# Kernel tuning notes

Hardware: AMD Instinct MI355X
Metric: run time of the kernel (lower is better)

Reference implementation:

```python
import jax, jax.numpy as jnp
import numpy as np

N, CIN, COUT, H, CH, K, M = 60000, 128, 128, 8, 16, 27, 960000


def setup_inputs() -> dict:
    key = jax.random.key(0)
    ks = jax.random.split(key, 12)
    f32 = jnp.float32
    s = 1.0 / np.sqrt(CIN)
    return {
        "feats": jax.random.normal(ks[0], (N, CIN), f32),
        "norm_points": jax.random.uniform(ks[1], (N, 3), f32) - 0.5,
        "w1": jax.random.normal(ks[2], (3, 3), f32) * 0.5,
        "bn1_scale": jnp.ones((3,), f32),
        "bn1_shift": jnp.zeros((3,), f32),
        "w2": jax.random.normal(ks[3], (3, CIN), f32) * 0.5,
        "bn2_scale": jnp.ones((CIN,), f32),
        "bn2_shift": jnp.zeros((CIN,), f32),
        "w3": jax.random.normal(ks[4], (CIN, CIN), f32) * s,
        "b3": jnp.zeros((CIN,), f32),
        "wq": jax.random.normal(ks[5], (CIN, COUT), f32) * s,
        "bq": jnp.zeros((COUT,), f32),
        "wv": jax.random.normal(ks[6], (CIN, COUT), f32) * s,
        "bv": jnp.zeros((COUT,), f32),
        "wo": jax.random.normal(ks[7], (COUT, COUT), f32) * s,
        "bo": jnp.zeros((COUT,), f32),
        "pos_enc": jax.random.normal(ks[8], (K, H, CH), f32),
        # kq_map row0 = key_idx * K + kernel_offset; row1 = query_idx
        "kq_row0": jax.random.randint(ks[9], (M,), 0, N * K, dtype=jnp.int32).astype(jnp.int64),
        "kq_row1": jax.random.randint(ks[10], (M,), 0, N, dtype=jnp.int32).astype(jnp.int64),
    }


def _l2norm(x):
    # F.normalize(p=2, dim=-1) with eps clamp
    n = jnp.linalg.norm(x, axis=-1, keepdims=True)
    return x / jnp.maximum(n, 1e-12)


def reference(feats, norm_points, w1, bn1_scale, bn1_shift, w2, bn2_scale, bn2_shift,
              w3, b3, wq, bq, wv, bv, wo, bo, pos_enc, kq_row0, kq_row1):
    # intra-voxel positional MLP (BN folded to eval-mode scale/shift)
    h = jax.nn.relu((norm_points @ w1) * bn1_scale + bn1_shift)
    h = jax.nn.relu((h @ w2) * bn2_scale + bn2_shift)
    x = feats + (h @ w3 + b3)                      # [N, CIN]

    q = (x @ wq + bq).reshape(N, H, CH)            # [N, H, CH]
    v = (x @ wv + bv).reshape(N, H, CH)

    nq = _l2norm(q)                                # normalized queries
    npos = _l2norm(pos_enc)                        # [K, H, CH]

    koff = kq_row0 % K                             # kernel-offset index into pos_enc
    kidx = kq_row0 // K                            # key (value) index

    # dot_product_cuda: attn[m,h] = <nq[query_m], npos[offset_m]>
    attn = jnp.einsum('mhc,mhc->mh', nq[kq_row1], npos[koff])   # [M, H]

    # scalar_attention_cuda: out[query_m] += attn[m] * v[key_m]
    msg = attn[:, :, None] * v[kidx]                             # [M, H, CH]
    out = jax.ops.segment_sum(msg, kq_row1, num_segments=N)      # [N, H, CH]

    return out.reshape(N, COUT) @ wo + bo
```

## Files before the change

### kernel.cpp

```cpp
#include <hip/hip_runtime.h>
#include <hip/hip_bf16.h>

#define NPTS  60000
#define KK    27
#define NEDGE 960000
#define CAP   96

typedef __attribute__((ext_vector_type(8))) short bf16x8;
typedef __attribute__((ext_vector_type(4))) float f32x4;

__device__ __forceinline__ unsigned short f2bf(float x) {
    unsigned u = __float_as_uint(x);
    return (unsigned short)((u + 0x7FFFu + ((u >> 16) & 1u)) >> 16);
}

union U8 { bf16x8 v; unsigned u[4]; };

__device__ __forceinline__ void split8(float4 a, float4 b, bf16x8& hi, bf16x8& lo) {
    float av[8] = {a.x, a.y, a.z, a.w, b.x, b.y, b.z, b.w};
    U8 h, l;
#pragma unroll
    for (int p = 0; p < 4; ++p) {
        float x0 = av[2 * p], x1 = av[2 * p + 1];
        unsigned hp;
        asm("v_cvt_pk_bf16_f32 %0, %1, %2" : "=v"(hp) : "v"(x0), "v"(x1));
        float hf0 = __uint_as_float(hp << 16);
        float hf1 = __uint_as_float(hp & 0xFFFF0000u);
        float r0 = x0 - hf0, r1 = x1 - hf1;
        unsigned lp;
        asm("v_cvt_pk_bf16_f32 %0, %1, %2" : "=v"(lp) : "v"(r0), "v"(r1));
        h.u[p] = hp; l.u[p] = lp;
    }
    hi = h.v; lo = l.v;
}

__global__ __launch_bounds__(256) void tiny_mlp_kernel(
    const float* __restrict__ npnts,
    const float* __restrict__ w1, const float* __restrict__ bn1s, const float* __restrict__ bn1h,
    const float* __restrict__ w2, const float* __restrict__ bn2s, const float* __restrict__ bn2h,
    float* __restrict__ h2out) {
    __shared__ float w2s[3 * 128];
    __shared__ float sc2[128], sh2[128];
    __shared__ float w1s[9], sc1[3], sh1[3];
    __shared__ float h2s[64 * 129];

    const int tid = threadIdx.x;
    for (int i = tid; i < 384; i += 256) w2s[i] = w2[i];
    if (tid < 128) { sc2[tid] = bn2s[tid]; sh2[tid] = bn2h[tid]; }
    if (tid < 9) w1s[tid] = w1[tid];
    if (tid < 3) { sc1[tid] = bn1s[tid]; sh1[tid] = bn1h[tid]; }
    __syncthreads();

    const int p  = tid >> 2;
    const int cq = (tid & 3) * 32;
    const int pt = blockIdx.x * 64 + p;
    float h1a = 0.f, h1b = 0.f, h1c = 0.f;
    if (pt < NPTS) {
        float p0 = npnts[pt * 3 + 0], p1 = npnts[pt * 3 + 1], p2 = npnts[pt * 3 + 2];
        float t0 = p0 * w1s[0] + p1 * w1s[3] + p2 * w1s[6];
        float t1 = p0 * w1s[1] + p1 * w1s[4] + p2 * w1s[7];
        float t2 = p0 * w1s[2] + p1 * w1s[5] + p2 * w1s[8];
        h1a = fmaxf(t0 * sc1[0] + sh1[0], 0.f);
        h1b = fmaxf(t1 * sc1[1] + sh1[1], 0.f);
        h1c = fmaxf(t2 * sc1[2] + sh1[2], 0.f);
    }
    for (int c = cq; c < cq + 32; ++c) {
        float t = h1a * w2s[c] + h1b * w2s[128 + c] + h1c * w2s[256 + c];
        h2s[p * 129 + c] = fmaxf(t * sc2[c] + sh2[c], 0.f);
    }
    __syncthreads();
    for (int i = tid; i < 64 * 128; i += 256) {
        int row = i >> 7, col = i & 127;
        int gr = blockIdx.x * 64 + row;
        if (gr < NPTS) h2out[gr * 128 + col] = h2s[row * 129 + col];
    }
}

__global__ __launch_bounds__(256) void pack_w_kernel(
    const float* __restrict__ w3, const float* __restrict__ wq,
    const float* __restrict__ wv, const float* __restrict__ wo,
    short* __restrict__ hi, short* __restrict__ lo) {
    const float* srcs[4] = {w3, wq, wv, wo};
    const float* w = srcs[blockIdx.y];
    short* whi = hi + blockIdx.y * 16384;
    short* wlo = lo + blockIdx.y * 16384;
    int base = (blockIdx.x * 256 + threadIdx.x) * 4;
#pragma unroll
    for (int j = 0; j < 4; ++j) {
        int o   = base + j;
        int s   = o & 7;
        int c16 = (o >> 3) & 15;
        int q   = (o >> 7) & 3;
        int t   = (o >> 9) & 7;
        int ks  = (o >> 12) & 3;
        float x = w[(ks * 32 + q * 8 + s) * 128 + (t * 16 + c16)];
        unsigned short h = f2bf(x);
        float hf = __uint_as_float((unsigned)h << 16);
        whi[o] = (short)h;
        wlo[o] = (short)f2bf(x - hf);
    }
}

template <int MODE>
__global__ __launch_bounds__(256, 2) void mfma_gemm_kernel(
    const float* __restrict__ in,
    const short* __restrict__ whi_g, const short* __restrict__ wlo_g,
    const float* __restrict__ bias, const float* __restrict__ resid,
    float* __restrict__ out) {
    const int tid  = threadIdx.x;
    const int lane = tid & 63;
    const int wv   = tid >> 6;
    const int q    = lane >> 4;
    const int cl   = lane & 15;
    const int rowbase = blockIdx.x * 128 + wv * 32;

    const bf16x8* BH = (const bf16x8*)whi_g;
    const bf16x8* BL = (const bf16x8*)wlo_g;
    const float* inA0 = &in[(size_t)min(rowbase + cl,      NPTS - 1) * 128];
    const float* inA1 = &in[(size_t)min(rowbase + 16 + cl, NPTS - 1) * 128];

    f32x4 acc[2][8];
#pragma unroll
    for (int u = 0; u < 2; ++u)
#pragma unroll
        for (int t = 0; t < 8; ++t) acc[u][t] = (f32x4){0.f, 0.f, 0.f, 0.f};

#pragma unroll
    for (int ks = 0; ks < 4; ++ks) {
        float4 a0a = *(const float4*)&inA0[ks * 32 + q * 8];
        float4 a0b = *(const float4*)&inA0[ks * 32 + q * 8 + 4];
        float4 a1a = *(const float4*)&inA1[ks * 32 + q * 8];
        float4 a1b = *(const float4*)&inA1[ks * 32 + q * 8 + 4];
        bf16x8 ah0, al0, ah1, al1;
        split8(a0a, a0b, ah0, al0);
        split8(a1a, a1b, ah1, al1);
#pragma unroll
        for (int t = 0; t < 8; ++t) {
            const int fi = ((ks * 8 + t) * 4 + q) * 16 + cl;
            bf16x8 bh = BH[fi];
            bf16x8 bl = BL[fi];
            acc[0][t] = __builtin_amdgcn_mfma_f32_16x16x32_bf16(ah0, bh, acc[0][t], 0, 0, 0);
            acc[0][t] = __builtin_amdgcn_mfma_f32_16x16x32_bf16(al0, bh, acc[0][t], 0, 0, 0);
            acc[0][t] = __builtin_amdgcn_mfma_f32_16x16x32_bf16(ah0, bl, acc[0][t], 0, 0, 0);
            acc[1][t] = __builtin_amdgcn_mfma_f32_16x16x32_bf16(ah1, bh, acc[1][t], 0, 0, 0);
            acc[1][t] = __builtin_amdgcn_mfma_f32_16x16x32_bf16(al1, bh, acc[1][t], 0, 0, 0);
            acc[1][t] = __builtin_amdgcn_mfma_f32_16x16x32_bf16(ah1, bl, acc[1][t], 0, 0, 0);
        }
    }

    float breg[8];
#pragma unroll
    for (int t = 0; t < 8; ++t) breg[t] = bias[t * 16 + cl];

#pragma unroll
    for (int u = 0; u < 2; ++u) {
#pragma unroll
        for (int t = 0; t < 8; ++t) {
#pragma unroll
            for (int r = 0; r < 4; ++r) {
                int row = rowbase + u * 16 + q * 4 + r;
                float o = acc[u][t][r] + breg[t];
                if (MODE == 1) {
                    if (row < NPTS) o += resid[row * 128 + t * 16 + cl];
                }
                if (MODE == 2) {
                    float ss = o * o;
                    ss += __shfl_xor(ss, 1);
                    ss += __shfl_xor(ss, 2);
                    ss += __shfl_xor(ss, 4);
                    ss += __shfl_xor(ss, 8);
                    o *= 1.f / fmaxf(sqrtf(ss), 1e-12f);
                }
                if (row < NPTS) out[row * 128 + t * 16 + cl] = o;
            }
        }
    }
}

__global__ __launch_bounds__(256) void zero_cnt_kernel(int* __restrict__ cnt) {
    int i = blockIdx.x * 256 + threadIdx.x;
    if (i < NPTS) cnt[i] = 0;
}

__global__ __launch_bounds__(256) void build_buckets_kernel(
    const int* __restrict__ r0, const int* __restrict__ r1,
    int* __restrict__ cnt, int* __restrict__ bucket) {
    int m = blockIdx.x * 256 + threadIdx.x;
    if (m >= NEDGE) return;
    int a = r0[m];
    int q = r1[m];
    if (q < 0 || q >= NPTS) return;
    if (a < 0 || a >= NPTS * KK) return;
    int kidx = a / KK;
    int koff = a - kidx * KK;
    int slot = atomicAdd(&cnt[q], 1);
    if (slot < CAP) bucket[q * CAP + slot] = (kidx << 5) | koff;
}

__global__ __launch_bounds__(256, 8) void attn_scatter_kernel(
    const float* __restrict__ nq, const float* __restrict__ v,
    const float* __restrict__ pos_enc, const int* __restrict__ cnt,
    const int* __restrict__ bucket, float* __restrict__ pre) {
    __shared__ float nps[KK * 128];

    const int tid = threadIdx.x;
    if (tid < KK * 8) {
        const float4* pv = (const float4*)&pos_enc[tid * 16];
        float4 a = pv[0], b = pv[1], c = pv[2], d = pv[3];
        float ss = a.x*a.x + a.y*a.y + a.z*a.z + a.w*a.w
                 + b.x*b.x + b.y*b.y + b.z*b.z + b.w*b.w
                 + c.x*c.x + c.y*c.y + c.z*c.z + c.w*c.w
                 + d.x*d.x + d.y*d.y + d.z*d.z + d.w*d.w;
        float inv = 1.f / fmaxf(sqrtf(ss), 1e-12f);
        float4* o = (float4*)&nps[tid * 16];
        o[0] = make_float4(a.x*inv, a.y*inv, a.z*inv, a.w*inv);
        o[1] = make_float4(b.x*inv, b.y*inv, b.z*inv, b.w*inv);
        o[2] = make_float4(c.x*inv, c.y*inv, c.z*inv, c.w*inv);
        o[3] = make_float4(d.x*inv, d.y*inv, d.z*inv, d.w*inv);
    }
    __syncthreads();

    const int l = tid & 63;
    const int wid = blockIdx.x * 4 + (tid >> 6);
    const int nwaves = gridDim.x * 4;

#define ATT_EDGE(REC) do {                                                  \
        int koff_ = (REC) & 31; int kidx_ = (REC) >> 5;                     \
        float2 np_ = *(const float2*)&nps[koff_ * 128 + 2 * l];             \
        float2 v_  = *(const float2*)&v[kidx_ * 128 + 2 * l];               \
        float a_ = nq2.x * np_.x + nq2.y * np_.y;                           \
        a_ += __shfl_xor(a_, 1); a_ += __shfl_xor(a_, 2);                   \
        a_ += __shfl_xor(a_, 4);                                            \
        accx = fmaf(a_, v_.x, accx); accy = fmaf(a_, v_.y, accy);           \
    } while (0)

    for (int n = wid; n < NPTS; n += nwaves) {
        float2 nq2 = *(const float2*)&nq[n * 128 + 2 * l];
        int deg = min(cnt[n], CAP);
        int base = n * CAP;
        int myrec = (l < deg) ? bucket[base + l] : 0;
        float accx = 0.f, accy = 0.f;
        int dmain = min(deg, 64);
        int e = 0;
        for (; e + 4 <= dmain; e += 4) {
            int r0 = __shfl(myrec, e);
            int r1 = __shfl(myrec, e + 1);
            int r2 = __shfl(myrec, e + 2);
            int r3 = __shfl(myrec, e + 3);
            ATT_EDGE(r0); ATT_EDGE(r1); ATT_EDGE(r2); ATT_EDGE(r3);
        }
        for (; e < dmain; ++e) {
            int r = __shfl(myrec, e);
            ATT_EDGE(r);
        }
        for (; e < deg; ++e) {
            int r = bucket[base + e];
            ATT_EDGE(r);
        }
        *(float2*)&pre[n * 128 + 2 * l] = make_float2(accx, accy);
    }
#undef ATT_EDGE
}

extern "C" void kernel_launch(void* const* d_in, const int* in_sizes, int n_in,
                              void* d_out, int out_size, void* d_ws, size_t ws_size,
                              hipStream_t stream) {
    const float* feats = (const float*)d_in[0];
    const float* npnts = (const float*)d_in[1];
    const float* w1    = (const float*)d_in[2];
    const float* bn1s  = (const float*)d_in[3];
    const float* bn1h  = (const float*)d_in[4];
    const float* w2    = (const float*)d_in[5];
    const float* bn2s  = (const float*)d_in[6];
    const float* bn2h  = (const float*)d_in[7];
    const float* w3    = (const float*)d_in[8];
    const float* b3    = (const float*)d_in[9];
    const float* wq    = (const float*)d_in[10];
    const float* bq    = (const float*)d_in[11];
    const float* wv    = (const float*)d_in[12];
    const float* bv    = (const float*)d_in[13];
    const float* wo    = (const float*)d_in[14];
    const float* bo    = (const float*)d_in[15];
    const float* pos   = (const float*)d_in[16];
    const int*   r0    = (const int*)d_in[17];
    const int*   r1    = (const int*)d_in[18];
    float* out = (float*)d_out;

    float* h2buf = (float*)d_ws;
    float* xbuf  = h2buf + (size_t)NPTS * 128;
    float* nqbuf = xbuf  + (size_t)NPTS * 128;
    float* vbuf  = nqbuf + (size_t)NPTS * 128;
    short* whi_g = (short*)(vbuf + (size_t)NPTS * 128);
    short* wlo_g = whi_g + 4 * 16384;
    float* prebuf = xbuf;
    int*   cnt    = (int*)h2buf;
    int*   bucket = cnt + NPTS;

    dim3 blk(256);
    const int nb64  = (NPTS + 63) / 64;
    const int nb128 = (NPTS + 127) / 128;

    pack_w_kernel<<<dim3(16, 4), blk, 0, stream>>>(w3, wq, wv, wo, whi_g, wlo_g);
    tiny_mlp_kernel<<<nb64, blk, 0, stream>>>(npnts, w1, bn1s, bn1h, w2, bn2s, bn2h, h2buf);
    mfma_gemm_kernel<1><<<nb128, blk, 0, stream>>>(h2buf, whi_g,             wlo_g,             b3, feats, xbuf);
    mfma_gemm_kernel<2><<<nb128, blk, 0, stream>>>(xbuf,  whi_g + 16384,     wlo_g + 16384,     bq, nullptr, nqbuf);
    mfma_gemm_kernel<0><<<nb128, blk, 0, stream>>>(xbuf,  whi_g + 2 * 16384, wlo_g + 2 * 16384, bv, nullptr, vbuf);
    zero_cnt_kernel<<<(NPTS + 255) / 256, blk, 0, stream>>>(cnt);
    build_buckets_kernel<<<(NEDGE + 255) / 256, blk, 0, stream>>>(r0, r1, cnt, bucket);
    attn_scatter_kernel<<<2048, blk, 0, stream>>>(nqbuf, vbuf, pos, cnt, bucket, prebuf);
    mfma_gemm_kernel<0><<<nb128, blk, 0, stream>>>(prebuf, whi_g + 3 * 16384, wlo_g + 3 * 16384, bo, nullptr, out);
}
```

Measured before the change: 387.4 us.

## Fuse positional MLP into x GEMM, merge q/v GEMMs, combine prep kernels

The positional MLP now writes its output into shared memory and feeds the residual GEMM in the same kernel, so the h2 intermediate no longer round-trips through global memory. The q and v projections become one kernel that reads x once and computes both outputs. Weight packing and count zeroing are merged into a single prep launch, which removes launches and re-reads of x in exchange for more registers per thread in the combined q/v kernel.

```diff
diff --git a/kernel.cpp b/kernel.cpp
--- a/kernel.cpp
+++ b/kernel.cpp
@@ -34,15 +34,50 @@
     hi = h.v; lo = l.v;
 }
 
-__global__ __launch_bounds__(256) void tiny_mlp_kernel(
+__global__ __launch_bounds__(256) void prep_kernel(
+    const float* __restrict__ w3, const float* __restrict__ wq,
+    const float* __restrict__ wv, const float* __restrict__ wo,
+    short* __restrict__ hi, short* __restrict__ lo, int* __restrict__ cnt) {
+    const int b = blockIdx.x;
+    const int tid = threadIdx.x;
+    if (b < 64) {
+        const float* srcs[4] = {w3, wq, wv, wo};
+        const int mat = b >> 4;
+        const float* w = srcs[mat];
+        short* whi = hi + mat * 16384;
+        short* wlo = lo + mat * 16384;
+        int base = ((b & 15) * 256 + tid) * 4;
+#pragma unroll
+        for (int j = 0; j < 4; ++j) {
+            int o   = base + j;
+            int s   = o & 7;
+            int c16 = (o >> 3) & 15;
+            int q   = (o >> 7) & 3;
+            int t   = (o >> 9) & 7;
+            int ks  = (o >> 12) & 3;
+            float x = w[(ks * 32 + q * 8 + s) * 128 + (t * 16 + c16)];
+            unsigned short h = f2bf(x);
+            float hf = __uint_as_float((unsigned)h << 16);
+            whi[o] = (short)h;
+            wlo[o] = (short)f2bf(x - hf);
+        }
+    } else {
+        int i = (b - 64) * 256 + tid;
+        if (i < NPTS) cnt[i] = 0;
+    }
+}
+
+__global__ __launch_bounds__(256, 2) void xgemm_mlp_kernel(
     const float* __restrict__ npnts,
     const float* __restrict__ w1, const float* __restrict__ bn1s, const float* __restrict__ bn1h,
     const float* __restrict__ w2, const float* __restrict__ bn2s, const float* __restrict__ bn2h,
-    float* __restrict__ h2out) {
+    const short* __restrict__ whi_g, const short* __restrict__ wlo_g,
+    const float* __restrict__ b3, const float* __restrict__ feats,
+    float* __restrict__ xout) {
+    __shared__ float h2s[64][132];
     __shared__ float w2s[3 * 128];
     __shared__ float sc2[128], sh2[128];
     __shared__ float w1s[9], sc1[3], sh1[3];
-    __shared__ float h2s[64 * 129];
 
     const int tid = threadIdx.x;
     for (int i = tid; i < 384; i += 256) w2s[i] = w2[i];
@@ -51,62 +86,146 @@
     if (tid < 3) { sc1[tid] = bn1s[tid]; sh1[tid] = bn1h[tid]; }
     __syncthreads();
 
-    const int p  = tid >> 2;
-    const int cq = (tid & 3) * 32;
-    const int pt = blockIdx.x * 64 + p;
-    float h1a = 0.f, h1b = 0.f, h1c = 0.f;
-    if (pt < NPTS) {
-        float p0 = npnts[pt * 3 + 0], p1 = npnts[pt * 3 + 1], p2 = npnts[pt * 3 + 2];
-        float t0 = p0 * w1s[0] + p1 * w1s[3] + p2 * w1s[6];
-        float t1 = p0 * w1s[1] + p1 * w1s[4] + p2 * w1s[7];
-        float t2 = p0 * w1s[2] + p1 * w1s[5] + p2 * w1s[8];
-        h1a = fmaxf(t0 * sc1[0] + sh1[0], 0.f);
-        h1b = fmaxf(t1 * sc1[1] + sh1[1], 0.f);
-        h1c = fmaxf(t2 * sc1[2] + sh1[2], 0.f);
-    }
-    for (int c = cq; c < cq + 32; ++c) {
-        float t = h1a * w2s[c] + h1b * w2s[128 + c] + h1c * w2s[256 + c];
-        h2s[p * 129 + c] = fmaxf(t * sc2[c] + sh2[c], 0.f);
+    {
+        const int p  = tid >> 2;
+        const int cq = (tid & 3) * 32;
+        const int pt = blockIdx.x * 64 + p;
+        float h1a = 0.f, h1b = 0.f, h1c = 0.f;
+        if (pt < NPTS) {
+            float p0 = npnts[pt * 3 + 0], p1 = npnts[pt * 3 + 1], p2 = npnts[pt * 3 + 2];
+            float t0 = p0 * w1s[0] + p1 * w1s[3] + p2 * w1s[6];
+            float t1 = p0 * w1s[1] + p1 * w1s[4] + p2 * w1s[7];
+            float t2 = p0 * w1s[2] + p1 * w1s[5] + p2 * w1s[8];
+            h1a = fmaxf(t0 * sc1[0] + sh1[0], 0.f);
+            h1b = fmaxf(t1 * sc1[1] + sh1[1], 0.f);
+            h1c = fmaxf(t2 * sc1[2] + sh1[2], 0.f);
+        }
+        for (int c = cq; c < cq + 32; ++c) {
+            float t = h1a * w2s[c] + h1b * w2s[128 + c] + h1c * w2s[256 + c];
+            h2s[p][c] = fmaxf(t * sc2[c] + sh2[c], 0.f);
+        }
     }
     __syncthreads();
-    for (int i = tid; i < 64 * 128; i += 256) {
-        int row = i >> 7, col = i & 127;
-        int gr = blockIdx.x * 64 + row;
-        if (gr < NPTS) h2out[gr * 128 + col] = h2s[row * 129 + col];
-    }
-}
-
-__global__ __launch_bounds__(256) void pack_w_kernel(
-    const float* __restrict__ w3, const float* __restrict__ wq,
-    const float* __restrict__ wv, const float* __restrict__ wo,
-    short* __restrict__ hi, short* __restrict__ lo) {
-    const float* srcs[4] = {w3, wq, wv, wo};
-    const float* w = srcs[blockIdx.y];
-    short* whi = hi + blockIdx.y * 16384;
-    short* wlo = lo + blockIdx.y * 16384;
-    int base = (blockIdx.x * 256 + threadIdx.x) * 4;
-#pragma unroll
-    for (int j = 0; j < 4; ++j) {
-        int o   = base + j;
-        int s   = o & 7;
-        int c16 = (o >> 3) & 15;
-        int q   = (o >> 7) & 3;
-        int t   = (o >> 9) & 7;
-        int ks  = (o >> 12) & 3;
-        float x = w[(ks * 32 + q * 8 + s) * 128 + (t * 16 + c16)];
-        unsigned short h = f2bf(x);
-        float hf = __uint_as_float((unsigned)h << 16);
-        whi[o] = (short)h;
-        wlo[o] = (short)f2bf(x - hf);
-    }
-}
-
-template <int MODE>
+
+    const int lane = tid & 63;
+    const int wv   = tid >> 6;
+    const int q    = lane >> 4;
+    const int cl   = lane & 15;
+    const int row0 = blockIdx.x * 64 + wv * 16;
+    const int trow = wv * 16 + cl;
+
+    const bf16x8* BH = (const bf16x8*)whi_g;
+    const bf16x8* BL = (const bf16x8*)wlo_g;
+
+    f32x4 acc[8];
+#pragma unroll
+    for (int t = 0; t < 8; ++t) acc[t] = (f32x4){0.f, 0.f, 0.f, 0.f};
+
+#pragma unroll
+    for (int ks = 0; ks < 4; ++ks) {
+        float4 aa = *(const float4*)&h2s[trow][ks * 32 + q * 8];
+        float4 ab = *(const float4*)&h2s[trow][ks * 32 + q * 8 + 4];
+        bf16x8 ah, al;
+        split8(aa, ab, ah, al);
+#pragma unroll
+        for (int t = 0; t < 8; ++t) {
+            const int fi = ((ks * 8 + t) * 4 + q) * 16 + cl;
+            bf16x8 bh = BH[fi];
+            bf16x8 bl = BL[fi];
+            acc[t] = __builtin_amdgcn_mfma_f32_16x16x32_bf16(ah, bh, acc[t], 0, 0, 0);
+            acc[t] = __builtin_amdgcn_mfma_f32_16x16x32_bf16(al, bh, acc[t], 0, 0, 0);
+            acc[t] = __builtin_amdgcn_mfma_f32_16x16x32_bf16(ah, bl, acc[t], 0, 0, 0);
+        }
+    }
+
+#pragma unroll
+    for (int t = 0; t < 8; ++t) {
+        float bv_ = b3[t * 16 + cl];
+#pragma unroll
+        for (int r = 0; r < 4; ++r) {
+            int row = row0 + q * 4 + r;
+            if (row < NPTS) {
+                float o = acc[t][r] + bv_ + feats[row * 128 + t * 16 + cl];
+                xout[row * 128 + t * 16 + cl] = o;
+            }
+        }
+    }
+}
+
+__global__ __launch_bounds__(256, 2) void mfma_gemm_qv_kernel(
+    const float* __restrict__ in,
+    const short* __restrict__ whq, const short* __restrict__ wlq,
+    const short* __restrict__ whv, const short* __restrict__ wlv,
+    const float* __restrict__ bq, const float* __restrict__ bv,
+    float* __restrict__ nqout, float* __restrict__ vout) {
+    const int tid  = threadIdx.x;
+    const int lane = tid & 63;
+    const int wv   = tid >> 6;
+    const int q    = lane >> 4;
+    const int cl   = lane & 15;
+    const int row0 = blockIdx.x * 64 + wv * 16;
+    const int arow = min(row0 + cl, NPTS - 1);
+
+    const bf16x8* QH = (const bf16x8*)whq;
+    const bf16x8* QL = (const bf16x8*)wlq;
+    const bf16x8* VH = (const bf16x8*)whv;
+    const bf16x8* VL = (const bf16x8*)wlv;
+    const float*  A  = &in[(size_t)arow * 128];
+
+    f32x4 accq[8], accv[8];
+#pragma unroll
+    for (int t = 0; t < 8; ++t) {
+        accq[t] = (f32x4){0.f, 0.f, 0.f, 0.f};
+        accv[t] = (f32x4){0.f, 0.f, 0.f, 0.f};
+    }
+
+#pragma unroll
+    for (int ks = 0; ks < 4; ++ks) {
+        float4 aa = *(const float4*)&A[ks * 32 + q * 8];
+        float4 ab = *(const float4*)&A[ks * 32 + q * 8 + 4];
+        bf16x8 ah, al;
+        split8(aa, ab, ah, al);
+#pragma unroll
+        for (int t = 0; t < 8; ++t) {
+            const int fi = ((ks * 8 + t) * 4 + q) * 16 + cl;
+            bf16x8 qh = QH[fi], ql = QL[fi];
+            bf16x8 vh = VH[fi], vl = VL[fi];
+            accq[t] = __builtin_amdgcn_mfma_f32_16x16x32_bf16(ah, qh, accq[t], 0, 0, 0);
+            accq[t] = __builtin_amdgcn_mfma_f32_16x16x32_bf16(al, qh, accq[t], 0, 0, 0);
+            accq[t] = __builtin_amdgcn_mfma_f32_16x16x32_bf16(ah, ql, accq[t], 0, 0, 0);
+            accv[t] = __builtin_amdgcn_mfma_f32_16x16x32_bf16(ah, vh, accv[t], 0, 0, 0);
+            accv[t] = __builtin_amdgcn_mfma_f32_16x16x32_bf16(al, vh, accv[t], 0, 0, 0);
+            accv[t] = __builtin_amdgcn_mfma_f32_16x16x32_bf16(ah, vl, accv[t], 0, 0, 0);
+        }
+    }
+
+#pragma unroll
+    for (int t = 0; t < 8; ++t) {
+        float bq_ = bq[t * 16 + cl];
+        float bv_ = bv[t * 16 + cl];
+#pragma unroll
+        for (int r = 0; r < 4; ++r) {
+            int row = row0 + q * 4 + r;
+            float oq = accq[t][r] + bq_;
+            float ov = accv[t][r] + bv_;
+            float ss = oq * oq;
+            ss += __shfl_xor(ss, 1);
+            ss += __shfl_xor(ss, 2);
+            ss += __shfl_xor(ss, 4);
+            ss += __shfl_xor(ss, 8);
+            oq *= 1.f / fmaxf(sqrtf(ss), 1e-12f);
+            if (row < NPTS) {
+                nqout[row * 128 + t * 16 + cl] = oq;
+                vout[row * 128 + t * 16 + cl]  = ov;
+            }
+        }
+    }
+}
+
 __global__ __launch_bounds__(256, 2) void mfma_gemm_kernel(
     const float* __restrict__ in,
     const short* __restrict__ whi_g, const short* __restrict__ wlo_g,
-    const float* __restrict__ bias, const float* __restrict__ resid,
-    float* __restrict__ out) {
+    const float* __restrict__ bias, float* __restrict__ out) {
     const int tid  = threadIdx.x;
     const int lane = tid & 63;
     const int wv   = tid >> 6;
@@ -159,27 +278,10 @@
 #pragma unroll
             for (int r = 0; r < 4; ++r) {
                 int row = rowbase + u * 16 + q * 4 + r;
-                float o = acc[u][t][r] + breg[t];
-                if (MODE == 1) {
-                    if (row < NPTS) o += resid[row * 128 + t * 16 + cl];
-                }
-                if (MODE == 2) {
-                    float ss = o * o;
-                    ss += __shfl_xor(ss, 1);
-                    ss += __shfl_xor(ss, 2);
-                    ss += __shfl_xor(ss, 4);
-                    ss += __shfl_xor(ss, 8);
-                    o *= 1.f / fmaxf(sqrtf(ss), 1e-12f);
-                }
-                if (row < NPTS) out[row * 128 + t * 16 + cl] = o;
+                if (row < NPTS) out[row * 128 + t * 16 + cl] = acc[u][t][r] + breg[t];
             }
         }
     }
-}
-
-__global__ __launch_bounds__(256) void zero_cnt_kernel(int* __restrict__ cnt) {
-    int i = blockIdx.x * 256 + threadIdx.x;
-    if (i < NPTS) cnt[i] = 0;
 }
 
 __global__ __launch_bounds__(256) void build_buckets_kernel(
@@ -286,27 +388,27 @@
     const int*   r1    = (const int*)d_in[18];
     float* out = (float*)d_out;
 
-    float* h2buf = (float*)d_ws;
-    float* xbuf  = h2buf + (size_t)NPTS * 128;
+    float* xbuf  = (float*)d_ws;
     float* nqbuf = xbuf  + (size_t)NPTS * 128;
     float* vbuf  = nqbuf + (size_t)NPTS * 128;
     short* whi_g = (short*)(vbuf + (size_t)NPTS * 128);
     short* wlo_g = whi_g + 4 * 16384;
+    int*   cnt    = (int*)(wlo_g + 4 * 16384);
+    int*   bucket = cnt + NPTS;
     float* prebuf = xbuf;
-    int*   cnt    = (int*)h2buf;
-    int*   bucket = cnt + NPTS;
 
     dim3 blk(256);
     const int nb64  = (NPTS + 63) / 64;
     const int nb128 = (NPTS + 127) / 128;
-
-    pack_w_kernel<<<dim3(16, 4), blk, 0, stream>>>(w3, wq, wv, wo, whi_g, wlo_g);
-    tiny_mlp_kernel<<<nb64, blk, 0, stream>>>(npnts, w1, bn1s, bn1h, w2, bn2s, bn2h, h2buf);
-    mfma_gemm_kernel<1><<<nb128, blk, 0, stream>>>(h2buf, whi_g,             wlo_g,             b3, feats, xbuf);
-    mfma_gemm_kernel<2><<<nb128, blk, 0, stream>>>(xbuf,  whi_g + 16384,     wlo_g + 16384,     bq, nullptr, nqbuf);
-    mfma_gemm_kernel<0><<<nb128, blk, 0, stream>>>(xbuf,  whi_g + 2 * 16384, wlo_g + 2 * 16384, bv, nullptr, vbuf);
-    zero_cnt_kernel<<<(NPTS + 255) / 256, blk, 0, stream>>>(cnt);
+    const int nprep = 64 + (NPTS + 255) / 256;
+
+    prep_kernel<<<nprep, blk, 0, stream>>>(w3, wq, wv, wo, whi_g, wlo_g, cnt);
+    xgemm_mlp_kernel<<<nb64, blk, 0, stream>>>(npnts, w1, bn1s, bn1h, w2, bn2s, bn2h,
+                                               whi_g, wlo_g, b3, feats, xbuf);
+    mfma_gemm_qv_kernel<<<nb64, blk, 0, stream>>>(xbuf,
+        whi_g + 16384, wlo_g + 16384, whi_g + 2 * 16384, wlo_g + 2 * 16384,
+        bq, bv, nqbuf, vbuf);
     build_buckets_kernel<<<(NEDGE + 255) / 256, blk, 0, stream>>>(r0, r1, cnt, bucket);
     attn_scatter_kernel<<<2048, blk, 0, stream>>>(nqbuf, vbuf, pos, cnt, bucket, prebuf);
-    mfma_gemm_kernel<0><<<nb128, blk, 0, stream>>>(prebuf, whi_g + 3 * 16384, wlo_g + 3 * 16384, bo, nullptr, out);
-}
+    mfma_gemm_kernel<<<nb128, blk, 0, stream>>>(prebuf, whi_g + 3 * 16384, wlo_g + 3 * 16384, bo, out);
+}
```

Result: faster. 353.3 us (-8.8%).
